# Performance work log

Measured on AMD Instinct MI355X. Metric: run time of the kernel, lower is better.

Reference implementation:

```python
import jax, jax.numpy as jnp
import numpy as np

D_MODEL, D_K, D_V, H = 512, 64, 64, 8
B, NQ, NK = 4, 2048, 2048


def setup_inputs() -> dict:
    key = jax.random.key(0)
    ks = jax.random.split(key, 14)
    s = 0.02
    return {
        "queries": jax.random.normal(ks[0], (B, NQ, D_MODEL), jnp.float32),
        "keys": jax.random.normal(ks[1], (B, NK, D_MODEL), jnp.float32),
        "values": jax.random.normal(ks[2], (B, NK, D_MODEL), jnp.float32),
        "attention_weights": jax.random.uniform(ks[3], (B, H, NQ, NK), jnp.float32),
        "attention_mask": jax.random.bernoulli(ks[4], 0.1, (B, H, NQ, NK)),
        "Wq": jax.random.normal(ks[5], (D_MODEL, H * D_K), jnp.float32) * s,
        "bq": jnp.zeros((H * D_K,), jnp.float32),
        "Wk": jax.random.normal(ks[6], (D_MODEL, H * D_K), jnp.float32) * s,
        "bk": jnp.zeros((H * D_K,), jnp.float32),
        "Wv": jax.random.normal(ks[7], (D_MODEL, H * D_V), jnp.float32) * s,
        "bv": jnp.zeros((H * D_V,), jnp.float32),
        "Wo": jax.random.normal(ks[8], (H * D_V, D_MODEL), jnp.float32) * s,
        "bo": jnp.zeros((D_MODEL,), jnp.float32),
    }


def reference(queries, keys, values, attention_weights, attention_mask,
              Wq, bq, Wk, bk, Wv, bv, Wo, bo):
    b_s, nq, _ = queries.shape
    nk = keys.shape[1]
    # projections -> (b, h, seq, d)
    q = (queries @ Wq + bq).reshape(b_s, nq, H, D_K).transpose(0, 2, 1, 3)
    k = (keys @ Wk + bk).reshape(b_s, nk, H, D_K).transpose(0, 2, 1, 3)
    v = (values @ Wv + bv).reshape(b_s, nk, H, D_V).transpose(0, 2, 1, 3)
    scale = 1.0 / np.sqrt(D_K).astype(np.float32)
    att = jnp.einsum("bhqd,bhkd->bhqk", q, k) * scale
    att = att * attention_weights
    att = jnp.where(attention_mask, -jnp.inf, att)
    att = jax.nn.softmax(att, axis=-1)
    out = jnp.einsum("bhqk,bhkd->bhqd", att, v)
    out = out.transpose(0, 2, 1, 3).reshape(b_s, nq, H * D_V)
    return out @ Wo + bo
```

## Files before the change

### kernel.cpp

```cpp
#include <hip/hip_runtime.h>
#include <hip/hip_bf16.h>
#include <math.h>

#define B_   4
#define H_   8
#define NQ_  2048
#define NK_  2048
#define DM_  512
#define DK_  64
#define WL_  262144

typedef short  bf16x8 __attribute__((ext_vector_type(8)));
typedef float  f32x4  __attribute__((ext_vector_type(4)));

static __device__ __forceinline__ f32x4 MFMA16(bf16x8 a, bf16x8 b, f32x4 c) {
    return __builtin_amdgcn_mfma_f32_16x16x32_bf16(a, b, c, 0, 0, 0);
}
static __device__ __forceinline__ unsigned short f2bf(float f) {
    __hip_bfloat16 h = __float2bfloat16(f);
    unsigned short u; __builtin_memcpy(&u, &h, 2); return u;
}
static __device__ __forceinline__ float bf2f(unsigned short u) {
    unsigned int x = ((unsigned int)u) << 16;
    float f; __builtin_memcpy(&f, &x, 4); return f;
}
static __device__ __forceinline__ void glds16(const void* g, void* l) {
    __builtin_amdgcn_global_load_lds(
        (__attribute__((address_space(1))) const void*)g,
        (__attribute__((address_space(3))) void*)l, 16, 0, 0);
}

__global__ __launch_bounds__(256) void conv_mask(const unsigned char* __restrict__ Mk,
                                                 unsigned long long* __restrict__ bits)
{
    __shared__ int s_flag;
    const int tid = threadIdx.x;
    if (tid == 0) s_flag = 0;
    __syncthreads();
    {
        bool any = false;
#pragma unroll
        for (int i = 1; i < 16; i += 4)
            if (Mk[tid*16 + i]) any = true;
        if (any) s_flag = 1;
    }
    __syncthreads();

    const long long NELEM = (long long)B_*H_*NQ_*NK_;
    const long long nth   = (long long)gridDim.x * 256;
    const long long T     = (long long)blockIdx.x * 256 + tid;
    unsigned short* b16   = (unsigned short*)bits;
    const uint4*    src   = (const uint4*)Mk;

    if (s_flag) {
        const long long n = NELEM / 16;
        for (long long t = T; t < n; t += nth) {
            const uint4 u = src[t];
            const unsigned int w[4] = {u.x, u.y, u.z, u.w};
            unsigned int m = 0;
#pragma unroll
            for (int j = 0; j < 4; ++j)
#pragma unroll
                for (int b2 = 0; b2 < 4; ++b2)
                    if ((w[j] >> (8*b2)) & 0xffu) m |= 1u << (4*j + b2);
            b16[t] = (unsigned short)m;
        }
    } else {
        const long long n = NELEM / 4;
        const int l3 = tid & 3;
        for (long long t = T; t < n; t += nth) {
            const uint4 u = src[t];
            const unsigned int nib = (u.x ? 1u : 0u) | (u.y ? 2u : 0u) |
                                     (u.z ? 4u : 0u) | (u.w ? 8u : 0u);
            unsigned int v = nib << (4*l3);
            v |= __shfl_xor(v, 1, 64);
            v |= __shfl_xor(v, 2, 64);
            if (l3 == 0) b16[t >> 2] = (unsigned short)v;
        }
    }
}

__global__ __launch_bounds__(256) void wprep(const float* __restrict__ Wq,
                                             const float* __restrict__ Wk,
                                             const float* __restrict__ Wv,
                                             const float* __restrict__ Wo,
                                             unsigned short* __restrict__ out)
{
    __shared__ float tile[64][65];
    const int tid = threadIdx.x;
    const int k0 = blockIdx.x * 64, n0 = blockIdx.y * 64, w = blockIdx.z;
    const float* W = (w == 0) ? Wq : (w == 1) ? Wk : (w == 2) ? Wv : Wo;
    unsigned short* WTh = out + (size_t)w * 2 * WL_;
    unsigned short* WTl = WTh + WL_;

#pragma unroll
    for (int rd = 0; rd < 4; ++rd) {
        const int k = (tid >> 4) + 16*rd, c4 = (tid & 15) * 4;
        const float4 v4 = *(const float4*)(W + (size_t)(k0 + k)*DM_ + n0 + c4);
        tile[k][c4+0] = v4.x; tile[k][c4+1] = v4.y;
        tile[k][c4+2] = v4.z; tile[k][c4+3] = v4.w;
    }
    __syncthreads();
#pragma unroll
    for (int rd = 0; rd < 4; ++rd) {
        const int n = (tid >> 4) + 16*rd, kk = (tid & 15) * 4;
        unsigned short hh[4], ll[4];
#pragma unroll
        for (int j = 0; j < 4; ++j) {
            const float f = tile[kk + j][n];
            hh[j] = f2bf(f);
            ll[j] = f2bf(f - bf2f(hh[j]));
        }
        *(ushort4*)(WTh + (size_t)(n0 + n)*DM_ + k0 + kk) = make_ushort4(hh[0],hh[1],hh[2],hh[3]);
        *(ushort4*)(WTl + (size_t)(n0 + n)*DM_ + k0 + kk) = make_ushort4(ll[0],ll[1],ll[2],ll[3]);
    }
}

template<int MODE>
__global__ __launch_bounds__(256) void gemm_split(
    const float* __restrict__ A,
    const unsigned short* __restrict__ WTh,
    const unsigned short* __restrict__ WTl,
    const float* __restrict__ bias,
    void* __restrict__ outv, const float oscale)
{
    __shared__ unsigned short Ah[64][64], Al[64][64], Bh[64][64], Bl[64][64];

    const int tid = threadIdx.x;
    const int w = tid >> 6, lane = tid & 63, g = lane >> 4, r = lane & 15;
    const int m0 = blockIdx.x * 64, n0 = blockIdx.y * 64;

    char* pAh = (char*)&Ah[0][0];
    char* pAl = (char*)&Al[0][0];
    char* pBh = (char*)&Bh[0][0];
    char* pBl = (char*)&Bl[0][0];

    const f32x4 z4 = {0.f, 0.f, 0.f, 0.f};
    f32x4 acc[4] = {z4, z4, z4, z4};

    for (int kt = 0; kt < DM_; kt += 64) {
#pragma unroll
        for (int rd = 0; rd < 4; ++rd) {
            const int row = (tid >> 4) + 16*rd;
            const int c4  = (tid & 15) * 4;
            const float4 a4 = *(const float4*)(A + (size_t)(m0 + row)*DM_ + kt + c4);
            const float av[4] = {a4.x, a4.y, a4.z, a4.w};
            unsigned short hh[4];
#pragma unroll
            for (int j = 0; j < 4; ++j) hh[j] = f2bf(av[j]);
            const int bo = (c4 * 2) ^ ((row & 7) << 4);
            *(ushort4*)(pAh + row*128 + bo) = make_ushort4(hh[0],hh[1],hh[2],hh[3]);
            if (MODE == 2) {
                unsigned short ll[4];
#pragma unroll
                for (int j = 0; j < 4; ++j) ll[j] = f2bf(av[j] - bf2f(hh[j]));
                *(ushort4*)(pAl + row*128 + bo) = make_ushort4(ll[0],ll[1],ll[2],ll[3]);
            }
        }
#pragma unroll
        for (int rd = 0; rd < 2; ++rd) {
            const int idx = tid + 256*rd;
            const int row = idx >> 3;
            const int cb  = (idx & 7) * 16;
            const int bo  = cb ^ ((row & 7) << 4);
            const size_t goff = (size_t)(n0 + row)*DM_ + kt + (cb >> 1);
            *(bf16x8*)(pBh + row*128 + bo) = *(const bf16x8*)(WTh + goff);
            *(bf16x8*)(pBl + row*128 + bo) = *(const bf16x8*)(WTl + goff);
        }
        __syncthreads();

        const int swr = (r & 7) << 4;
#pragma unroll
        for (int ks = 0; ks < 2; ++ks) {
            const int xo = (64*ks + 16*g) ^ swr;
            const bf16x8 xh = *(const bf16x8*)(pAh + (16*w + r)*128 + xo);
#pragma unroll
            for (int nt = 0; nt < 4; ++nt) {
                const bf16x8 bh = *(const bf16x8*)(pBh + (16*nt + r)*128 + xo);
                const bf16x8 bl = *(const bf16x8*)(pBl + (16*nt + r)*128 + xo);
                if (MODE == 1) {
                    acc[nt] = MFMA16(xh, bh, acc[nt]);
                    acc[nt] = MFMA16(xh, bl, acc[nt]);
                } else if (MODE == 0) {
                    acc[nt] = MFMA16(bh, xh, acc[nt]);
                    acc[nt] = MFMA16(bl, xh, acc[nt]);
                } else {
                    const bf16x8 xl = *(const bf16x8*)(pAl + (16*w + r)*128 + xo);
                    acc[nt] = MFMA16(bh, xh, acc[nt]);
                    acc[nt] = MFMA16(bh, xl, acc[nt]);
                    acc[nt] = MFMA16(bl, xh, acc[nt]);
                }
            }
        }
        __syncthreads();
    }

    if (MODE == 0) {
        const int m = m0 + 16*w + r;
        const int b = m >> 11, q = m & 2047, h = blockIdx.y;
        unsigned short* dst = (unsigned short*)outv + (((size_t)(b*H_ + h))*NQ_ + q)*DK_;
#pragma unroll
        for (int nt = 0; nt < 4; ++nt) {
            unsigned short u[4];
#pragma unroll
            for (int j = 0; j < 4; ++j)
                u[j] = f2bf((acc[nt][j] + bias[n0 + 16*nt + 4*g + j]) * oscale);
            *(ushort4*)(dst + 16*nt + 4*g) = make_ushort4(u[0],u[1],u[2],u[3]);
        }
    } else if (MODE == 1) {
        const int b = m0 >> 11, h = blockIdx.y;
        const int key = (m0 & 2047) + 16*w + 4*g;
#pragma unroll
        for (int nt = 0; nt < 4; ++nt) {
            const int dv = 16*nt + r;
            const float bv = bias[n0 + dv];
            unsigned short u[4];
#pragma unroll
            for (int j = 0; j < 4; ++j) u[j] = f2bf(acc[nt][j] + bv);
            *(ushort4*)((unsigned short*)outv +
                        (((size_t)(b*H_ + h))*DK_ + dv)*NK_ + key) = make_ushort4(u[0],u[1],u[2],u[3]);
        }
    } else {
        const int m = m0 + 16*w + r;
        float* dst = (float*)outv + (size_t)m*DM_ + n0;
#pragma unroll
        for (int nt = 0; nt < 4; ++nt) {
            float4 o4;
            o4.x = acc[nt][0] + bias[n0 + 16*nt + 4*g + 0];
            o4.y = acc[nt][1] + bias[n0 + 16*nt + 4*g + 1];
            o4.z = acc[nt][2] + bias[n0 + 16*nt + 4*g + 2];
            o4.w = acc[nt][3] + bias[n0 + 16*nt + 4*g + 3];
            *(float4*)(dst + 16*nt + 4*g) = o4;
        }
    }
}

__global__ __launch_bounds__(256, 4) void attn_mfma(
    const unsigned short* __restrict__ Qb,
    const unsigned short* __restrict__ Kb,
    const unsigned short* __restrict__ Vt,
    const float* __restrict__ Wt,
    const unsigned long long* __restrict__ Mb,
    float* __restrict__ O)
{
    __shared__ unsigned short KT[64][64];
    __shared__ unsigned short VTs[64][64];
    __shared__ float          WT[64][64];
    __shared__ short          Pl[4][1024];

    const int tid  = threadIdx.x;
    const int wv   = tid >> 6, lane = tid & 63;
    const int g    = lane >> 4, r = lane & 15;
    const int q0   = blockIdx.x * 64 + wv * 16;
    const int bh   = blockIdx.y;

    const size_t kvBase = (size_t)bh * NK_ * DK_;
    const unsigned short* qp = Qb + kvBase + (size_t)(q0 + r)*DK_ + 8*g;
    const bf16x8 qf0 = *(const bf16x8*)qp;
    const bf16x8 qf1 = *(const bf16x8*)(qp + 32);

    const float* wblock = Wt + ((size_t)bh*NQ_ + blockIdx.x*64)*NK_;
    const unsigned long long* brow = Mb + ((size_t)bh*NQ_ + q0 + r)*(NK_/64);
    const unsigned short* kg = Kb + kvBase;
    const unsigned short* vg = Vt + kvBase;

    const f32x4 zero4 = {0.f, 0.f, 0.f, 0.f};
    f32x4 oa0 = zero4, oa1 = zero4, oa2 = zero4, oa3 = zero4;
    float m_run = -1e30f, l_run = 0.f;

    char* pbase = (char*)&Pl[wv][0];
    const int roff = r * 128;
    const int sw   = (r & 7) << 4;

    const int kv_soff = 8 * ((lane & 7) ^ (lane >> 3));
    const int kv_r8   = lane >> 3;
    const int w_r4    = lane >> 4;

#pragma unroll 1
    for (int i = 0; i < 32; ++i) {
        const int kt = i * 64;

#pragma unroll
        for (int c = 0; c < 2; ++c) {
            const int rowl = 16*wv + c*8 + kv_r8;
            glds16(kg + (size_t)(kt + rowl)*DK_ + kv_soff,
                   &KT[16*wv + c*8][0] + lane*8);
            glds16(vg + (size_t)rowl*NK_ + kt + kv_soff,
                   &VTs[16*wv + c*8][0] + lane*8);
        }
#pragma unroll
        for (int c = 0; c < 4; ++c) {
            const int rowl = 16*wv + c*4 + w_r4;
            glds16(wblock + (size_t)rowl*NK_ + kt + 4*((lane & 15) ^ (c*4 + w_r4)),
                   &WT[16*wv + c*4][0] + lane*4);
        }
        const unsigned long long bcur = brow[i];
        __syncthreads();

        f32x4 sa0 = zero4, sa1 = zero4, sa2 = zero4, sa3 = zero4;
        {
            const bf16x8 k00 = *(const bf16x8*)&KT[ 0 + r][8*((g    ) ^ (r & 7))];
            const bf16x8 k01 = *(const bf16x8*)&KT[ 0 + r][8*((g + 4) ^ (r & 7))];
            const bf16x8 k10 = *(const bf16x8*)&KT[16 + r][8*((g    ) ^ (r & 7))];
            const bf16x8 k11 = *(const bf16x8*)&KT[16 + r][8*((g + 4) ^ (r & 7))];
            const bf16x8 k20 = *(const bf16x8*)&KT[32 + r][8*((g    ) ^ (r & 7))];
            const bf16x8 k21 = *(const bf16x8*)&KT[32 + r][8*((g + 4) ^ (r & 7))];
            const bf16x8 k30 = *(const bf16x8*)&KT[48 + r][8*((g    ) ^ (r & 7))];
            const bf16x8 k31 = *(const bf16x8*)&KT[48 + r][8*((g + 4) ^ (r & 7))];
            sa0 = MFMA16(k00, qf0, sa0); sa0 = MFMA16(k01, qf1, sa0);
            sa1 = MFMA16(k10, qf0, sa1); sa1 = MFMA16(k11, qf1, sa1);
            sa2 = MFMA16(k20, qf0, sa2); sa2 = MFMA16(k21, qf1, sa2);
            sa3 = MFMA16(k30, qf0, sa3); sa3 = MFMA16(k31, qf1, sa3);
        }

        f32x4 wf[4];
#pragma unroll
        for (int t = 0; t < 4; ++t)
            wf[t] = *(const f32x4*)&WT[16*wv + r][4*((4*t + g) ^ r)];

        float lg[16];
        const f32x4 sav[4] = {sa0, sa1, sa2, sa3};
#pragma unroll
        for (int t = 0; t < 4; ++t) {
            const unsigned int half = (t & 2) ? (unsigned int)(bcur >> 32)
                                              : (unsigned int)bcur;
#pragma unroll
            for (int j = 0; j < 4; ++j) {
                const unsigned int bit = (half >> (16*(t & 1) + 4*g + j)) & 1u;
                lg[4*t+j] = bit ? -1e30f : sav[t][j] * wf[t][j];
            }
        }

        float mx = lg[0];
#pragma unroll
        for (int i2 = 1; i2 < 16; ++i2) mx = fmaxf(mx, lg[i2]);
        mx = fmaxf(mx, __shfl_xor(mx, 16, 64));
        mx = fmaxf(mx, __shfl_xor(mx, 32, 64));
        const float mnew = fmaxf(m_run, mx);
        const float fsc  = __expf(m_run - mnew);
        m_run = mnew;
        float p16[16], rs = 0.f;
#pragma unroll
        for (int i2 = 0; i2 < 16; ++i2) { p16[i2] = __expf(lg[i2] - mnew); rs += p16[i2]; }
        rs += __shfl_xor(rs, 16, 64);
        rs += __shfl_xor(rs, 32, 64);
        l_run = l_run * fsc + rs;

#pragma unroll
        for (int t = 0; t < 4; ++t) {
            const unsigned int w0 = (unsigned int)f2bf(p16[4*t+0]) |
                                    ((unsigned int)f2bf(p16[4*t+1]) << 16);
            const unsigned int w1 = (unsigned int)f2bf(p16[4*t+2]) |
                                    ((unsigned int)f2bf(p16[4*t+3]) << 16);
            *(int2*)(pbase + roff + ((32*t + 8*g) ^ sw)) = make_int2((int)w0, (int)w1);
        }
        const bf16x8 pa0 = *(const bf16x8*)(pbase + roff + ((     16*g) ^ sw));
        const bf16x8 pa1 = *(const bf16x8*)(pbase + roff + ((64 + 16*g) ^ sw));

        float fr[4];
#pragma unroll
        for (int j = 0; j < 4; ++j) fr[j] = __shfl(fsc, 4*g + j, 64);
#pragma unroll
        for (int j = 0; j < 4; ++j) {
            oa0[j] *= fr[j]; oa1[j] *= fr[j]; oa2[j] *= fr[j]; oa3[j] *= fr[j];
        }

        {
            const bf16x8 v00 = *(const bf16x8*)&VTs[ 0 + r][8*((g    ) ^ (r & 7))];
            const bf16x8 v01 = *(const bf16x8*)&VTs[16 + r][8*((g    ) ^ (r & 7))];
            const bf16x8 v02 = *(const bf16x8*)&VTs[32 + r][8*((g    ) ^ (r & 7))];
            const bf16x8 v03 = *(const bf16x8*)&VTs[48 + r][8*((g    ) ^ (r & 7))];
            const bf16x8 v10 = *(const bf16x8*)&VTs[ 0 + r][8*((g + 4) ^ (r & 7))];
            const bf16x8 v11 = *(const bf16x8*)&VTs[16 + r][8*((g + 4) ^ (r & 7))];
            const bf16x8 v12 = *(const bf16x8*)&VTs[32 + r][8*((g + 4) ^ (r & 7))];
            const bf16x8 v13 = *(const bf16x8*)&VTs[48 + r][8*((g + 4) ^ (r & 7))];
            oa0 = MFMA16(pa0, v00, oa0); oa1 = MFMA16(pa0, v01, oa1);
            oa2 = MFMA16(pa0, v02, oa2); oa3 = MFMA16(pa0, v03, oa3);
            oa0 = MFMA16(pa1, v10, oa0); oa1 = MFMA16(pa1, v11, oa1);
            oa2 = MFMA16(pa1, v12, oa2); oa3 = MFMA16(pa1, v13, oa3);
        }
        __syncthreads();
    }

    const float inv = 1.0f / l_run;
    float ir[4];
#pragma unroll
    for (int j = 0; j < 4; ++j) ir[j] = __shfl(inv, 4*g + j, 64);
    const int bb = bh >> 3, h = bh & 7;
    const f32x4 oav[4] = {oa0, oa1, oa2, oa3};
#pragma unroll
    for (int nt = 0; nt < 4; ++nt)
#pragma unroll
        for (int j = 0; j < 4; ++j)
            O[((size_t)(bb*NQ_ + q0 + 4*g + j))*DM_ + h*64 + 16*nt + r] = oav[nt][j] * ir[j];
}

extern "C" void kernel_launch(void* const* d_in, const int* in_sizes, int n_in,
                              void* d_out, int out_size, void* d_ws, size_t ws_size,
                              hipStream_t stream) {
    (void)in_sizes; (void)n_in; (void)out_size; (void)ws_size;

    const float* q    = (const float*)d_in[0];
    const float* k    = (const float*)d_in[1];
    const float* v    = (const float*)d_in[2];
    const float* attw = (const float*)d_in[3];
    const unsigned char* mask = (const unsigned char*)d_in[4];
    const float* Wq = (const float*)d_in[5];
    const float* bq = (const float*)d_in[6];
    const float* Wk = (const float*)d_in[7];
    const float* bk = (const float*)d_in[8];
    const float* Wv = (const float*)d_in[9];
    const float* bv = (const float*)d_in[10];
    const float* Wo = (const float*)d_in[11];
    const float* bo = (const float*)d_in[12];
    float* out = (float*)d_out;

    const long long NE = (long long)B_*H_*NQ_*DK_;
    unsigned short* q_bf = (unsigned short*)d_ws;
    unsigned short* k_bf = q_bf + NE;
    unsigned short* vT   = q_bf + 2*NE;
    unsigned short* wt   = q_bf + 3*NE;
    unsigned long long* bits = (unsigned long long*)(wt + 8LL*WL_);
    const long long NB = (long long)B_*H_*NQ_*NK_/64;
    float* o_ws = (float*)(bits + NB);

    const dim3 blk(256);
    wprep<<<dim3(8, 8, 4), blk, 0, stream>>>(Wq, Wk, Wv, Wo, wt);
    conv_mask<<<dim3(2048), blk, 0, stream>>>(mask, bits);

    const dim3 gg(128, 8);
    gemm_split<0><<<gg, blk, 0, stream>>>(q, wt + 0*WL_, wt + 1*WL_, bq, q_bf, 0.125f);
    gemm_split<0><<<gg, blk, 0, stream>>>(k, wt + 2*WL_, wt + 3*WL_, bk, k_bf, 1.0f);
    gemm_split<1><<<gg, blk, 0, stream>>>(v, wt + 4*WL_, wt + 5*WL_, bv, vT, 1.0f);

    attn_mfma<<<dim3(NQ_/64, B_*H_), blk, 0, stream>>>(q_bf, k_bf, vT, attw, bits, o_ws);

    gemm_split<2><<<gg, blk, 0, stream>>>(o_ws, wt + 6*WL_, wt + 7*WL_, bo, out, 1.0f);
}
```

Measured before the change: 395.5 us.

## Double-buffer K, V and weight tiles in the attention loop

Doubles the LDS tiles for K, V and the attention-weight block. The next key tile is now issued asynchronously at the top of each iteration, while the current tile is being computed, and the barrier before compute is dropped. This aims to hide global-to-LDS load latency behind the MFMA and softmax work. In exchange, LDS use per block roughly doubles, and launch bounds drop from 4 to 2 blocks per CU, which lowers the occupancy available to hide latency in other ways.

New measurement: 405.0 us. 2.4% more time.

```diff
diff --git a/kernel.cpp b/kernel.cpp
--- a/kernel.cpp
+++ b/kernel.cpp
@@ -235,7 +235,7 @@
     }
 }
 
-__global__ __launch_bounds__(256, 4) void attn_mfma(
+__global__ __launch_bounds__(256, 2) void attn_mfma(
     const unsigned short* __restrict__ Qb,
     const unsigned short* __restrict__ Kb,
     const unsigned short* __restrict__ Vt,
@@ -243,9 +243,9 @@
     const unsigned long long* __restrict__ Mb,
     float* __restrict__ O)
 {
-    __shared__ unsigned short KT[64][64];
-    __shared__ unsigned short VTs[64][64];
-    __shared__ float          WT[64][64];
+    __shared__ unsigned short KT[2][64][64];
+    __shared__ unsigned short VTs[2][64][64];
+    __shared__ float          WT[2][64][64];
     __shared__ short          Pl[4][1024];
 
     const int tid  = threadIdx.x;
@@ -276,37 +276,44 @@
     const int kv_r8   = lane >> 3;
     const int w_r4    = lane >> 4;
 
-#pragma unroll 1
-    for (int i = 0; i < 32; ++i) {
+    auto stage = [&](int pbuf, int i) {
         const int kt = i * 64;
-
 #pragma unroll
         for (int c = 0; c < 2; ++c) {
             const int rowl = 16*wv + c*8 + kv_r8;
             glds16(kg + (size_t)(kt + rowl)*DK_ + kv_soff,
-                   &KT[16*wv + c*8][0] + lane*8);
+                   &KT[pbuf][16*wv + c*8][0] + lane*8);
             glds16(vg + (size_t)rowl*NK_ + kt + kv_soff,
-                   &VTs[16*wv + c*8][0] + lane*8);
+                   &VTs[pbuf][16*wv + c*8][0] + lane*8);
         }
 #pragma unroll
         for (int c = 0; c < 4; ++c) {
             const int rowl = 16*wv + c*4 + w_r4;
             glds16(wblock + (size_t)rowl*NK_ + kt + 4*((lane & 15) ^ (c*4 + w_r4)),
-                   &WT[16*wv + c*4][0] + lane*4);
-        }
+                   &WT[pbuf][16*wv + c*4][0] + lane*4);
+        }
+    };
+
+    stage(0, 0);
+    __syncthreads();
+
+#pragma unroll 1
+    for (int i = 0; i < 32; ++i) {
+        const int p = i & 1;
+
+        if (i + 1 < 32) stage(p ^ 1, i + 1);
         const unsigned long long bcur = brow[i];
-        __syncthreads();
 
         f32x4 sa0 = zero4, sa1 = zero4, sa2 = zero4, sa3 = zero4;
         {
-            const bf16x8 k00 = *(const bf16x8*)&KT[ 0 + r][8*((g    ) ^ (r & 7))];
-            const bf16x8 k01 = *(const bf16x8*)&KT[ 0 + r][8*((g + 4) ^ (r & 7))];
-            const bf16x8 k10 = *(const bf16x8*)&KT[16 + r][8*((g    ) ^ (r & 7))];
-            const bf16x8 k11 = *(const bf16x8*)&KT[16 + r][8*((g + 4) ^ (r & 7))];
-            const bf16x8 k20 = *(const bf16x8*)&KT[32 + r][8*((g    ) ^ (r & 7))];
-            const bf16x8 k21 = *(const bf16x8*)&KT[32 + r][8*((g + 4) ^ (r & 7))];
-            const bf16x8 k30 = *(const bf16x8*)&KT[48 + r][8*((g    ) ^ (r & 7))];
-            const bf16x8 k31 = *(const bf16x8*)&KT[48 + r][8*((g + 4) ^ (r & 7))];
+            const bf16x8 k00 = *(const bf16x8*)&KT[p][ 0 + r][8*((g    ) ^ (r & 7))];
+            const bf16x8 k01 = *(const bf16x8*)&KT[p][ 0 + r][8*((g + 4) ^ (r & 7))];
+            const bf16x8 k10 = *(const bf16x8*)&KT[p][16 + r][8*((g    ) ^ (r & 7))];
+            const bf16x8 k11 = *(const bf16x8*)&KT[p][16 + r][8*((g + 4) ^ (r & 7))];
+            const bf16x8 k20 = *(const bf16x8*)&KT[p][32 + r][8*((g    ) ^ (r & 7))];
+            const bf16x8 k21 = *(const bf16x8*)&KT[p][32 + r][8*((g + 4) ^ (r & 7))];
+            const bf16x8 k30 = *(const bf16x8*)&KT[p][48 + r][8*((g    ) ^ (r & 7))];
+            const bf16x8 k31 = *(const bf16x8*)&KT[p][48 + r][8*((g + 4) ^ (r & 7))];
             sa0 = MFMA16(k00, qf0, sa0); sa0 = MFMA16(k01, qf1, sa0);
             sa1 = MFMA16(k10, qf0, sa1); sa1 = MFMA16(k11, qf1, sa1);
             sa2 = MFMA16(k20, qf0, sa2); sa2 = MFMA16(k21, qf1, sa2);
@@ -316,7 +323,7 @@
         f32x4 wf[4];
 #pragma unroll
         for (int t = 0; t < 4; ++t)
-            wf[t] = *(const f32x4*)&WT[16*wv + r][4*((4*t + g) ^ r)];
+            wf[t] = *(const f32x4*)&WT[p][16*wv + r][4*((4*t + g) ^ r)];
 
         float lg[16];
         const f32x4 sav[4] = {sa0, sa1, sa2, sa3};
@@ -366,19 +373,20 @@
         }
 
         {
-            const bf16x8 v00 = *(const bf16x8*)&VTs[ 0 + r][8*((g    ) ^ (r & 7))];
-            const bf16x8 v01 = *(const bf16x8*)&VTs[16 + r][8*((g    ) ^ (r & 7))];
-            const bf16x8 v02 = *(const bf16x8*)&VTs[32 + r][8*((g    ) ^ (r & 7))];
-            const bf16x8 v03 = *(const bf16x8*)&VTs[48 + r][8*((g    ) ^ (r & 7))];
-            const bf16x8 v10 = *(const bf16x8*)&VTs[ 0 + r][8*((g + 4) ^ (r & 7))];
-            const bf16x8 v11 = *(const bf16x8*)&VTs[16 + r][8*((g + 4) ^ (r & 7))];
-            const bf16x8 v12 = *(const bf16x8*)&VTs[32 + r][8*((g + 4) ^ (r & 7))];
-            const bf16x8 v13 = *(const bf16x8*)&VTs[48 + r][8*((g + 4) ^ (r & 7))];
+            const bf16x8 v00 = *(const bf16x8*)&VTs[p][ 0 + r][8*((g    ) ^ (r & 7))];
+            const bf16x8 v01 = *(const bf16x8*)&VTs[p][16 + r][8*((g    ) ^ (r & 7))];
+            const bf16x8 v02 = *(const bf16x8*)&VTs[p][32 + r][8*((g    ) ^ (r & 7))];
+            const bf16x8 v03 = *(const bf16x8*)&VTs[p][48 + r][8*((g    ) ^ (r & 7))];
+            const bf16x8 v10 = *(const bf16x8*)&VTs[p][ 0 + r][8*((g + 4) ^ (r & 7))];
+            const bf16x8 v11 = *(const bf16x8*)&VTs[p][16 + r][8*((g + 4) ^ (r & 7))];
+            const bf16x8 v12 = *(const bf16x8*)&VTs[p][32 + r][8*((g + 4) ^ (r & 7))];
+            const bf16x8 v13 = *(const bf16x8*)&VTs[p][48 + r][8*((g + 4) ^ (r & 7))];
             oa0 = MFMA16(pa0, v00, oa0); oa1 = MFMA16(pa0, v01, oa1);
             oa2 = MFMA16(pa0, v02, oa2); oa3 = MFMA16(pa0, v03, oa3);
             oa0 = MFMA16(pa1, v10, oa0); oa1 = MFMA16(pa1, v11, oa1);
             oa2 = MFMA16(pa1, v12, oa2); oa3 = MFMA16(pa1, v13, oa3);
         }
+
         __syncthreads();
     }
 
```
